# Kernel optimization log

Measured on AMD Instinct MI355X. Metric: run time of the kernel, lower is better.

## Reference

```python
import jax, jax.numpy as jnp
import numpy as np

THRESH = 0.5
LENS = 0.5
DECAY = 0.5
CFG_FC = [256, 256, 256]
IN_SIZE = 1
OUT_SIZE = 10
T = 784 // IN_SIZE  # stride == input_size


def make_mask(dim, c_min, c_max, min_dc, max_dc, phase_shift_max, T=784):
    mask = []
    dc_steps = np.linspace(min_dc, max_dc, dim)
    cycles = np.linspace(c_min, c_max, dim)
    phase_shifts = np.linspace(0, int(phase_shift_max * c_max), dim)
    for cycle, dc, ps in zip(cycles, dc_steps, phase_shifts):
        cycle = int(np.ceil(cycle))
        on_length = int(np.ceil(dc * cycle))
        off_length = cycle - on_length
        pattern = [1] * on_length + [0] * off_length
        ps = int(np.round(ps))
        pattern = pattern[-ps:] + pattern[:-ps] if ps > 0 else pattern
        full_pattern = pattern * (T // cycle) + pattern[: T % cycle]
        mask.append(full_pattern)
    return jnp.asarray(np.array(mask, dtype=np.float32))  # [dim, T]


MASK1 = make_mask(CFG_FC[0], 4, 8, 0.1, 0.9, 0.5, T)
MASK2 = make_mask(CFG_FC[1], 4, 8, 0.1, 0.9, 0.5, T)
MASK3 = make_mask(CFG_FC[2], 4, 8, 0.1, 0.9, 0.5, T)


def act_fun(x):
    return (x > THRESH).astype(x.dtype)


def mem_update(x, mem, spike, mask):
    # mask: [H] broadcast over batch
    pre_mem = mem
    new_mem = mem * DECAY * (1.0 - spike) + x
    mem = jnp.where(mask == 0, pre_mem, new_mem)
    spike = act_fun(mem) * mask
    return mem, spike


def setup_inputs() -> dict:
    key = jax.random.key(0)
    ks = jax.random.split(key, 14)
    def lin(k, out_d, in_d):
        s = 1.0 / np.sqrt(in_d)
        return jax.random.uniform(k, (out_d, in_d), jnp.float32, -s, s)
    def bia(k, out_d, in_d):
        s = 1.0 / np.sqrt(in_d)
        return jax.random.uniform(k, (out_d,), jnp.float32, -s, s)
    H1, H2, H3 = CFG_FC
    return {
        "x": jax.random.uniform(ks[0], (512, 784), jnp.float32),
        "w_i2h1": lin(ks[1], H1, IN_SIZE), "b_i2h1": bia(ks[2], H1, IN_SIZE),
        "w_h2h1": lin(ks[3], H1, H1), "b_h2h1": bia(ks[4], H1, H1),
        "w_i2h2": lin(ks[5], H2, H1), "b_i2h2": bia(ks[6], H2, H1),
        "w_h2h2": lin(ks[7], H2, H2), "b_h2h2": bia(ks[8], H2, H2),
        "w_i2h3": lin(ks[9], H3, H2), "b_i2h3": bia(ks[10], H3, H2),
        "w_h2o3": lin(ks[11], OUT_SIZE, H3), "b_h2o3": bia(ks[12], OUT_SIZE, H3),
    }


def _build_x_seq(x):
    # replicate the torch slicing: start = step*stride, clamp to last window
    D = x.shape[1]
    starts = np.arange(T) * IN_SIZE
    starts = np.where(starts < T - IN_SIZE, starts, D - IN_SIZE)
    idx = starts[:, None] + np.arange(IN_SIZE)  # [T, in]
    x_seq = x[:, idx]                            # [N, T, in]
    return jnp.transpose(x_seq, (1, 0, 2))       # [T, N, in]


def reference(x, w_i2h1, b_i2h1, w_h2h1, b_h2h1, w_i2h2, b_i2h2,
              w_h2h2, b_h2h2, w_i2h3, b_i2h3, w_h2o3, b_h2o3):
    N = x.shape[0]
    H1, H2, H3 = CFG_FC
    x_seq = _build_x_seq(x)                       # [T, N, in]
    m1 = MASK1.T                                  # [T, H1]
    m2 = MASK2.T
    m3 = MASK3.T

    init = (jnp.zeros((N, H1)), jnp.zeros((N, H1)),
            jnp.zeros((N, H2)), jnp.zeros((N, H2)),
            jnp.zeros((N, H3)), jnp.zeros((N, H3)),
            jnp.zeros((N, OUT_SIZE)))

    def step(carry, inp):
        mem1, spk1, mem2, spk2, mem3, spk3, out_sum = carry
        xt, mk1, mk2, mk3 = inp
        h1 = xt @ w_i2h1.T + b_i2h1 + spk1 @ w_h2h1.T + b_h2h1
        mem1, spk1 = mem_update(h1, mem1, spk1, mk1)
        h2 = spk1 @ w_i2h2.T + b_i2h2 + spk2 @ w_h2h2.T + b_h2h2
        mem2, spk2 = mem_update(h2, mem2, spk2, mk2)
        h3 = spk2 @ w_i2h3.T + b_i2h3
        mem3, spk3 = mem_update(h3, mem3, spk3, mk3)
        out = spk3 @ w_h2o3.T + b_h2o3
        return (mem1, spk1, mem2, spk2, mem3, spk3, out_sum + out), None

    (final, _) = jax.lax.scan(step, init, (x_seq, m1, m2, m3))
    out_sum = final[-1]
    return out_sum / T
```

## Files before the change

### kernel.cpp

```cpp
#include <hip/hip_runtime.h>
#include <stdint.h>

#define T_STEPS 784
#define H 256
#define NBLK 256
#define NTHR 256

typedef unsigned long long u64;

__device__ __forceinline__ void mask_params(int j, int& c, int& on, int& ps) {
    const double stepc = (8.0 - 4.0) / 255.0;
    const double stepd = (0.9 - 0.1) / 255.0;
    const double stepp = 4.0 / 255.0;
    double cyc = (j == 255) ? 8.0 : __dadd_rn(__dmul_rn((double)j, stepc), 4.0);
    c = (int)ceil(cyc);
    double dc  = (j == 255) ? 0.9 : __dadd_rn(__dmul_rn((double)j, stepd), 0.1);
    on = (int)ceil(__dmul_rn(dc, (double)c));
    double psd = (j == 255) ? 4.0 : __dmul_rn((double)j, stepp);
    ps = (int)rint(psd);
}

__device__ __forceinline__ void fmac4(float4& a, float f, const float4& w) {
    a.x = fmaf(f, w.x, a.x); a.y = fmaf(f, w.y, a.y);
    a.z = fmaf(f, w.z, a.z); a.w = fmaf(f, w.w, a.w);
}

#define SELF(m,k) ((((m) >> (k)) & 1ull) ? 1.0f : 0.0f)

#define APPLY2(ki, xi, yi)                                         \
    {   float f0 = SELF(m0, ki), f1 = SELF(m1, ki);                \
        fmac4(aX0, f0, xi); fmac4(aX1, f1, xi);                    \
        fmac4(aY0, f0, yi); fmac4(aY1, f1, yi); }

__device__ __forceinline__ void consume_pair_2s(const char* __restrict__ bX,
                                                const char* __restrict__ bY,
                                                u64 m0, u64 m1, int l16,
                                                float4& aX0, float4& aX1,
                                                float4& aY0, float4& aY1) {
    u64 u = m0 | m1;
    int n = __popcll(u);
    while (n >= 8) {
        int k0=__builtin_ctzll(u); u&=u-1; int k1=__builtin_ctzll(u); u&=u-1;
        int k2=__builtin_ctzll(u); u&=u-1; int k3=__builtin_ctzll(u); u&=u-1;
        int k4=__builtin_ctzll(u); u&=u-1; int k5=__builtin_ctzll(u); u&=u-1;
        int k6=__builtin_ctzll(u); u&=u-1; int k7=__builtin_ctzll(u); u&=u-1;
        float4 x0 = *(const float4*)(bX + (k0<<10) + l16);
        float4 x1 = *(const float4*)(bX + (k1<<10) + l16);
        float4 x2 = *(const float4*)(bX + (k2<<10) + l16);
        float4 x3 = *(const float4*)(bX + (k3<<10) + l16);
        float4 x4 = *(const float4*)(bX + (k4<<10) + l16);
        float4 x5 = *(const float4*)(bX + (k5<<10) + l16);
        float4 x6 = *(const float4*)(bX + (k6<<10) + l16);
        float4 x7 = *(const float4*)(bX + (k7<<10) + l16);
        float4 y0 = *(const float4*)(bY + (k0<<10) + l16);
        float4 y1 = *(const float4*)(bY + (k1<<10) + l16);
        float4 y2 = *(const float4*)(bY + (k2<<10) + l16);
        float4 y3 = *(const float4*)(bY + (k3<<10) + l16);
        float4 y4 = *(const float4*)(bY + (k4<<10) + l16);
        float4 y5 = *(const float4*)(bY + (k5<<10) + l16);
        float4 y6 = *(const float4*)(bY + (k6<<10) + l16);
        float4 y7 = *(const float4*)(bY + (k7<<10) + l16);
        APPLY2(k0, x0, y0); APPLY2(k1, x1, y1);
        APPLY2(k2, x2, y2); APPLY2(k3, x3, y3);
        APPLY2(k4, x4, y4); APPLY2(k5, x5, y5);
        APPLY2(k6, x6, y6); APPLY2(k7, x7, y7);
        n -= 8;
    }
    if (n & 4) {
        int k0=__builtin_ctzll(u); u&=u-1; int k1=__builtin_ctzll(u); u&=u-1;
        int k2=__builtin_ctzll(u); u&=u-1; int k3=__builtin_ctzll(u); u&=u-1;
        float4 x0 = *(const float4*)(bX + (k0<<10) + l16);
        float4 x1 = *(const float4*)(bX + (k1<<10) + l16);
        float4 x2 = *(const float4*)(bX + (k2<<10) + l16);
        float4 x3 = *(const float4*)(bX + (k3<<10) + l16);
        float4 y0 = *(const float4*)(bY + (k0<<10) + l16);
        float4 y1 = *(const float4*)(bY + (k1<<10) + l16);
        float4 y2 = *(const float4*)(bY + (k2<<10) + l16);
        float4 y3 = *(const float4*)(bY + (k3<<10) + l16);
        APPLY2(k0, x0, y0); APPLY2(k1, x1, y1);
        APPLY2(k2, x2, y2); APPLY2(k3, x3, y3);
    }
    if (n & 2) {
        int k0=__builtin_ctzll(u); u&=u-1; int k1=__builtin_ctzll(u); u&=u-1;
        float4 x0 = *(const float4*)(bX + (k0<<10) + l16);
        float4 x1 = *(const float4*)(bX + (k1<<10) + l16);
        float4 y0 = *(const float4*)(bY + (k0<<10) + l16);
        float4 y1 = *(const float4*)(bY + (k1<<10) + l16);
        APPLY2(k0, x0, y0); APPLY2(k1, x1, y1);
    }
    if (n & 1) {
        int k0 = __builtin_ctzll(u);
        float4 x0 = *(const float4*)(bX + (k0<<10) + l16);
        float4 y0 = *(const float4*)(bY + (k0<<10) + l16);
        APPLY2(k0, x0, y0);
    }
}

__device__ __forceinline__ void upd(float& mem, float& sp, float h, int mbit) {
    float nm = fmaf(mem * 0.5f, (1.0f - sp), h);
    mem = mbit ? nm : mem;
    sp  = (mbit && (mem > 0.5f)) ? 1.0f : 0.0f;
}

__global__ __launch_bounds__(256)
void prep_transpose(const float* __restrict__ w1, const float* __restrict__ w2a,
                    const float* __restrict__ w2b, const float* __restrict__ w3,
                    float* __restrict__ ws)
{
    __shared__ float tile[64][65];
    const int bid = blockIdx.x;
    const int m  = bid >> 4;
    const int kt = (bid >> 2) & 3;
    const int jt = bid & 3;
    const float* src = (m == 0) ? w1 : (m == 1) ? w2a : (m == 2) ? w2b : w3;
    float* dst = ws + (size_t)m * H * H;
    const int tid = threadIdx.x;
    const int c = tid & 63, r4 = tid >> 6;
    #pragma unroll
    for (int rr = 0; rr < 16; rr++) {
        int r = r4 * 16 + rr;
        tile[r][c] = src[(size_t)(jt * 64 + r) * H + kt * 64 + c];
    }
    __syncthreads();
    #pragma unroll
    for (int rr = 0; rr < 16; rr++) {
        int r = r4 * 16 + rr;
        dst[(size_t)(kt * 64 + r) * H + jt * 64 + c] = tile[c][r];
    }
}

__global__ __launch_bounds__(NTHR, 2)
void srnn_kernel(const float* __restrict__ x,
                 const float* __restrict__ w_i2h1, const float* __restrict__ b_i2h1,
                 const float* __restrict__ b_h2h1,
                 const float* __restrict__ b_i2h2, const float* __restrict__ b_h2h2,
                 const float* __restrict__ b_i2h3,
                 const float* __restrict__ w_h2o3, const float* __restrict__ b_h2o3,
                 const float* __restrict__ ws,
                 float* __restrict__ out)
{
    const int tid  = threadIdx.x;
    const int lane = tid & 63;
    const int w    = tid >> 6;
    const int j    = tid;
    const int l16  = lane * 16;
    const int s0   = blockIdx.x * 2;

    const char* wt1  = (const char*)ws + (0 << 18) + (w << 16);
    const char* wt2a = (const char*)ws + (1 << 18) + (w << 16);
    const char* wt2b = (const char*)ws + (2 << 18) + (w << 16);
    const char* wt3  = (const char*)ws + (3 << 18) + (w << 16);

    __shared__ float pexA[2][2][4][H];
    __shared__ float pexB[2][2][4][H];
    __shared__ float pexC[2][2][4][H];
    __shared__ float wred[4][2][10];

    int mc, mon, mps;
    mask_params(j, mc, mon, mps);
    int ph = (mc - (mps % mc)) % mc;

    const float bs1 = b_i2h1[j] + b_h2h1[j];
    const float bs2 = b_i2h2[j] + b_h2h2[j];
    const float bs3 = b_i2h3[j];
    const float wi1 = w_i2h1[j];

    float mem1[2] = {0.f,0.f}, mem2[2] = {0.f,0.f}, mem3[2] = {0.f,0.f};
    float sp1 [2] = {0.f,0.f}, sp2 [2] = {0.f,0.f}, sp3 [2] = {0.f,0.f};
    u64 b1s0 = 0ull, b1s1 = 0ull;
    u64 b2s0 = 0ull, b2s1 = 0ull;
    int mb_d1 = 0, mb_d2 = 0;
    float cnt[2] = {0.f, 0.f};

    __syncthreads();

    for (int sl = 0; sl < T_STEPS + 2; sl++) {
        const int par  = sl & 1;
        const int mbit = (ph < mon) ? 1 : 0;
        const bool runL1 = (sl < T_STEPS);
        const bool runL2 = (sl >= 1) && (sl <= T_STEPS);
        const bool runL3 = (sl >= 2);

        float xq0 = 0.f, xq1 = 0.f;
        if (runL1) {
            xq0 = x[(size_t)s0 * T_STEPS + sl];
            xq1 = x[(size_t)(s0 + 1) * T_STEPS + sl];
        }

        float4 aA0={0,0,0,0}, aA1={0,0,0,0}, aBa0={0,0,0,0}, aBa1={0,0,0,0};
        float4 aBb0={0,0,0,0}, aBb1={0,0,0,0}, aC0={0,0,0,0}, aC1={0,0,0,0};
        consume_pair_2s(wt1,  wt2a, b1s0, b1s1, l16, aA0, aA1, aBa0, aBa1);
        consume_pair_2s(wt2b, wt3,  b2s0, b2s1, l16, aBb0, aBb1, aC0, aC1);
        float4 aB0, aB1;
        aB0.x = aBa0.x + aBb0.x; aB0.y = aBa0.y + aBb0.y;
        aB0.z = aBa0.z + aBb0.z; aB0.w = aBa0.w + aBb0.w;
        aB1.x = aBa1.x + aBb1.x; aB1.y = aBa1.y + aBb1.y;
        aB1.z = aBa1.z + aBb1.z; aB1.w = aBa1.w + aBb1.w;
        if (runL1) {
            ((float4*)pexA[par][0][w])[lane] = aA0;
            ((float4*)pexA[par][1][w])[lane] = aA1;
        }
        if (runL2) {
            ((float4*)pexB[par][0][w])[lane] = aB0;
            ((float4*)pexB[par][1][w])[lane] = aB1;
        }
        if (runL3) {
            ((float4*)pexC[par][0][w])[lane] = aC0;
            ((float4*)pexC[par][1][w])[lane] = aC1;
        }
        __syncthreads();

        if (runL1) {
            {
                float hs = (pexA[par][0][0][j] + pexA[par][0][1][j])
                         + (pexA[par][0][2][j] + pexA[par][0][3][j]);
                float h1 = hs + fmaf(xq0, wi1, bs1);
                upd(mem1[0], sp1[0], h1, mbit);
            }
            {
                float hs = (pexA[par][1][0][j] + pexA[par][1][1][j])
                         + (pexA[par][1][2][j] + pexA[par][1][3][j]);
                float h1 = hs + fmaf(xq1, wi1, bs1);
                upd(mem1[1], sp1[1], h1, mbit);
            }
            b1s0 = __ballot(sp1[0] != 0.0f);
            b1s1 = __ballot(sp1[1] != 0.0f);
        }
        if (runL2) {
            #pragma unroll
            for (int sp = 0; sp < 2; sp++) {
                float hs = (pexB[par][sp][0][j] + pexB[par][sp][1][j])
                         + (pexB[par][sp][2][j] + pexB[par][sp][3][j]);
                upd(mem2[sp], sp2[sp], hs + bs2, mb_d1);
            }
            b2s0 = __ballot(sp2[0] != 0.0f);
            b2s1 = __ballot(sp2[1] != 0.0f);
        }
        if (runL3) {
            #pragma unroll
            for (int sp = 0; sp < 2; sp++) {
                float hs = (pexC[par][sp][0][j] + pexC[par][sp][1][j])
                         + (pexC[par][sp][2][j] + pexC[par][sp][3][j]);
                upd(mem3[sp], sp3[sp], hs + bs3, mb_d2);
                cnt[sp] += sp3[sp];
            }
        }
        mb_d2 = mb_d1; mb_d1 = mbit;
        ph++; if (ph == mc) ph = 0;
    }

    #pragma unroll
    for (int i = 0; i < 10; i++) {
        float wo_i = w_h2o3[i * H + j];
        #pragma unroll
        for (int sp = 0; sp < 2; sp++) {
            float v = cnt[sp] * wo_i;
            for (int off = 32; off; off >>= 1) v += __shfl_down(v, off, 64);
            if (lane == 0) wred[w][sp][i] = v;
        }
    }
    __syncthreads();
    if (tid < 20) {
        int sp = tid / 10, i = tid % 10;
        float sum = (wred[0][sp][i] + wred[1][sp][i])
                  + (wred[2][sp][i] + wred[3][sp][i]);
        out[(size_t)(s0 + sp) * 10 + i] = sum / 784.0f + b_h2o3[i];
    }
}

extern "C" void kernel_launch(void* const* d_in, const int* in_sizes, int n_in,
                              void* d_out, int out_size, void* d_ws, size_t ws_size,
                              hipStream_t stream) {
    (void)in_sizes; (void)n_in; (void)ws_size; (void)out_size;
    const float* x      = (const float*)d_in[0];
    const float* w_i2h1 = (const float*)d_in[1];
    const float* b_i2h1 = (const float*)d_in[2];
    const float* w_h2h1 = (const float*)d_in[3];
    const float* b_h2h1 = (const float*)d_in[4];
    const float* w_i2h2 = (const float*)d_in[5];
    const float* b_i2h2 = (const float*)d_in[6];
    const float* w_h2h2 = (const float*)d_in[7];
    const float* b_h2h2 = (const float*)d_in[8];
    const float* w_i2h3 = (const float*)d_in[9];
    const float* b_i2h3 = (const float*)d_in[10];
    const float* w_h2o3 = (const float*)d_in[11];
    const float* b_h2o3 = (const float*)d_in[12];
    float* ws = (float*)d_ws;

    prep_transpose<<<64, 256, 0, stream>>>(w_h2h1, w_i2h2, w_h2h2, w_i2h3, ws);
    srnn_kernel<<<NBLK, NTHR, 0, stream>>>(x,
        w_i2h1, b_i2h1, b_h2h1,
        b_i2h2, b_h2h2, b_i2h3,
        w_h2o3, b_h2o3, ws,
        (float*)d_out);
}
```

Measured before the change: 2.103 ms.

## Split recurrent matvec across eight waves with half-wave neuron ownership

Doubles the block to 512 threads so each of the eight waves owns a 32-row slice of each weight matrix instead of 64. Each wave's partial sums go to shared memory and are reduced over 8 partials. Neuron state is owned by the lower 32 lanes of each wave, with ballots masked to 32 bits. The aim is to shorten the per-timestep serial matvec latency by spreading it over more waves. The cost is more shared memory, a wider reduction, duplicated upper-half lanes, and possibly lower occupancy or register pressure under the launch bounds.

```diff
diff --git a/kernel.cpp b/kernel.cpp
--- a/kernel.cpp
+++ b/kernel.cpp
@@ -4,7 +4,7 @@
 #define T_STEPS 784
 #define H 256
 #define NBLK 256
-#define NTHR 256
+#define NTHR 512
 
 typedef unsigned long long u64;
 
@@ -142,19 +142,19 @@
     const int tid  = threadIdx.x;
     const int lane = tid & 63;
     const int w    = tid >> 6;
-    const int j    = tid;
+    const int j    = w * 32 + (lane & 31);
     const int l16  = lane * 16;
     const int s0   = blockIdx.x * 2;
 
-    const char* wt1  = (const char*)ws + (0 << 18) + (w << 16);
-    const char* wt2a = (const char*)ws + (1 << 18) + (w << 16);
-    const char* wt2b = (const char*)ws + (2 << 18) + (w << 16);
-    const char* wt3  = (const char*)ws + (3 << 18) + (w << 16);
-
-    __shared__ float pexA[2][2][4][H];
-    __shared__ float pexB[2][2][4][H];
-    __shared__ float pexC[2][2][4][H];
-    __shared__ float wred[4][2][10];
+    const char* wt1  = (const char*)ws + (0 << 18) + (w << 15);
+    const char* wt2a = (const char*)ws + (1 << 18) + (w << 15);
+    const char* wt2b = (const char*)ws + (2 << 18) + (w << 15);
+    const char* wt3  = (const char*)ws + (3 << 18) + (w << 15);
+
+    __shared__ float pexA[2][2][8][H];
+    __shared__ float pexB[2][2][8][H];
+    __shared__ float pexC[2][2][8][H];
+    __shared__ float wred[8][2][10];
 
     int mc, mon, mps;
     mask_params(j, mc, mon, mps);
@@ -212,35 +212,43 @@
 
         if (runL1) {
             {
-                float hs = (pexA[par][0][0][j] + pexA[par][0][1][j])
-                         + (pexA[par][0][2][j] + pexA[par][0][3][j]);
+                float hs = ((pexA[par][0][0][j] + pexA[par][0][1][j])
+                          + (pexA[par][0][2][j] + pexA[par][0][3][j]))
+                         + ((pexA[par][0][4][j] + pexA[par][0][5][j])
+                          + (pexA[par][0][6][j] + pexA[par][0][7][j]));
                 float h1 = hs + fmaf(xq0, wi1, bs1);
                 upd(mem1[0], sp1[0], h1, mbit);
             }
             {
-                float hs = (pexA[par][1][0][j] + pexA[par][1][1][j])
-                         + (pexA[par][1][2][j] + pexA[par][1][3][j]);
+                float hs = ((pexA[par][1][0][j] + pexA[par][1][1][j])
+                          + (pexA[par][1][2][j] + pexA[par][1][3][j]))
+                         + ((pexA[par][1][4][j] + pexA[par][1][5][j])
+                          + (pexA[par][1][6][j] + pexA[par][1][7][j]));
                 float h1 = hs + fmaf(xq1, wi1, bs1);
                 upd(mem1[1], sp1[1], h1, mbit);
             }
-            b1s0 = __ballot(sp1[0] != 0.0f);
-            b1s1 = __ballot(sp1[1] != 0.0f);
+            b1s0 = __ballot(sp1[0] != 0.0f) & 0xFFFFFFFFull;
+            b1s1 = __ballot(sp1[1] != 0.0f) & 0xFFFFFFFFull;
         }
         if (runL2) {
             #pragma unroll
             for (int sp = 0; sp < 2; sp++) {
-                float hs = (pexB[par][sp][0][j] + pexB[par][sp][1][j])
-                         + (pexB[par][sp][2][j] + pexB[par][sp][3][j]);
+                float hs = ((pexB[par][sp][0][j] + pexB[par][sp][1][j])
+                          + (pexB[par][sp][2][j] + pexB[par][sp][3][j]))
+                         + ((pexB[par][sp][4][j] + pexB[par][sp][5][j])
+                          + (pexB[par][sp][6][j] + pexB[par][sp][7][j]));
                 upd(mem2[sp], sp2[sp], hs + bs2, mb_d1);
             }
-            b2s0 = __ballot(sp2[0] != 0.0f);
-            b2s1 = __ballot(sp2[1] != 0.0f);
+            b2s0 = __ballot(sp2[0] != 0.0f) & 0xFFFFFFFFull;
+            b2s1 = __ballot(sp2[1] != 0.0f) & 0xFFFFFFFFull;
         }
         if (runL3) {
             #pragma unroll
             for (int sp = 0; sp < 2; sp++) {
-                float hs = (pexC[par][sp][0][j] + pexC[par][sp][1][j])
-                         + (pexC[par][sp][2][j] + pexC[par][sp][3][j]);
+                float hs = ((pexC[par][sp][0][j] + pexC[par][sp][1][j])
+                          + (pexC[par][sp][2][j] + pexC[par][sp][3][j]))
+                         + ((pexC[par][sp][4][j] + pexC[par][sp][5][j])
+                          + (pexC[par][sp][6][j] + pexC[par][sp][7][j]));
                 upd(mem3[sp], sp3[sp], hs + bs3, mb_d2);
                 cnt[sp] += sp3[sp];
             }
@@ -255,15 +263,17 @@
         #pragma unroll
         for (int sp = 0; sp < 2; sp++) {
             float v = cnt[sp] * wo_i;
-            for (int off = 32; off; off >>= 1) v += __shfl_down(v, off, 64);
+            for (int off = 16; off; off >>= 1) v += __shfl_down(v, off, 32);
             if (lane == 0) wred[w][sp][i] = v;
         }
     }
     __syncthreads();
     if (tid < 20) {
         int sp = tid / 10, i = tid % 10;
-        float sum = (wred[0][sp][i] + wred[1][sp][i])
-                  + (wred[2][sp][i] + wred[3][sp][i]);
+        float sum = ((wred[0][sp][i] + wred[1][sp][i])
+                   + (wred[2][sp][i] + wred[3][sp][i]))
+                  + ((wred[4][sp][i] + wred[5][sp][i])
+                   + (wred[6][sp][i] + wred[7][sp][i]));
         out[(size_t)(s0 + sp) * 10 + i] = sum / 784.0f + b_h2o3[i];
     }
 }
```

After: 1.856 ms. 1.13x faster.
